# Optimization experiments

Hardware: AMD Instinct MI355X
Metric: run time of the kernel (lower is better)

## Reference

```python
import jax, jax.numpy as jnp
import numpy as np

# --- static configuration (mirrors init_kwargs) ---
L = 16        # latent_size
HL = 512      # hypernet_layer_size
D = 64        # decoder_layer_size
NDEC = 2      # decoder_n_layers
B, G = 128, 100  # batch, grid (pressure levels)
LOGP_MEAN, LOGP_STD = 0.0, 3.0
T_MEAN, T_STD = 1500.0, 500.0

# decoder layer structure generated by the hypernet
WEIGHT_SIZES = [(1, D)] + [(D, D)] * NDEC + [(D, 1)]
BIAS_SIZES = [1] + [D] * NDEC + [1]
OUT_SIZE = sum(a * b for a, b in WEIGHT_SIZES) + sum(BIAS_SIZES)  # 8450


def setup_inputs() -> dict:
    key = jax.random.key(0)
    ks = jax.random.split(key, 8)
    def init(k, shape, fan_in):
        return (jax.random.normal(k, shape, jnp.float32) / np.float32(np.sqrt(fan_in)))
    return {
        "z": jax.random.normal(ks[0], (B, L), jnp.float32),
        "log_P": jax.random.normal(ks[1], (B, G), jnp.float32) * 2.0,
        # hypernet MLP params: L -> HL -> HL -> HL -> OUT_SIZE
        "hW0": init(ks[2], (L, HL), L), "hb0": jnp.zeros((HL,), jnp.float32),
        "hW1": init(ks[3], (HL, HL), HL), "hb1": jnp.zeros((HL,), jnp.float32),
        "hW2": init(ks[4], (HL, HL), HL), "hb2": jnp.zeros((HL,), jnp.float32),
        "hWo": init(ks[5], (HL, OUT_SIZE), HL), "hbo": jnp.zeros((OUT_SIZE,), jnp.float32),
    }


def reference(z, log_P, hW0, hb0, hW1, hb1, hW2, hb2, hWo, hbo):
    Bsz, Gsz = log_P.shape
    R = Bsz * Gsz  # flattened rows
    # broadcast latent over the pressure grid: (B, L) -> (R, L)
    z_flat = jnp.broadcast_to(z[:, None, :], (Bsz, Gsz, z.shape[-1])).reshape(R, -1)
    # normalize pressure -> decoder input, shape (R, 1)
    x = (log_P.reshape(R, 1) - LOGP_MEAN) / LOGP_STD
    # hypernet MLP (leaky_relu, slope 0.01 like torch default)
    h = jax.nn.leaky_relu(z_flat @ hW0 + hb0)
    h = jax.nn.leaky_relu(h @ hW1 + hb1)
    h = jax.nn.leaky_relu(h @ hW2 + hb2)
    wab = h @ hWo + hbo  # (R, OUT_SIZE): per-row decoder weights+biases
    # per-row decoder: chain of batched GEMVs with siren activation
    off = 0
    n_layers = len(WEIGHT_SIZES)
    for i, ((di, do), bs) in enumerate(zip(WEIGHT_SIZES, BIAS_SIZES)):
        n = di * do
        w = wab[:, off:off + n].reshape(R, di, do)
        b = wab[:, off + n:off + n + bs]  # broadcasts against (R, do)
        off += n + bs
        x = jnp.einsum('bi,bij->bj', x, w) + b
        if i == 0:
            x = x * 30.0  # siren first-layer omega_0
        if i < n_layers - 1:
            x = jnp.sin(x)  # siren activation; last layer is Identity
    T_pred = x.reshape(Bsz, Gsz)
    # undo temperature normalization
    return T_pred * T_STD + T_MEAN
```

## Files before the change

kernel.cpp:

```cpp
#include <hip/hip_runtime.h>

#define WSTRIDE 8704
#define GSTR 65

__device__ __forceinline__ float lrelu(float x) { return x > 0.0f ? x : 0.01f * x; }

__global__ __launch_bounds__(128) void h0T_kernel(const float* __restrict__ z,
                                                  const float* __restrict__ W,
                                                  const float* __restrict__ bias,
                                                  float* __restrict__ h0T) {
    int j = blockIdx.x;
    int b = threadIdx.x;
    float zr[16];
    *(float4*)&zr[0]  = *(const float4*)&z[b * 16 + 0];
    *(float4*)&zr[4]  = *(const float4*)&z[b * 16 + 4];
    *(float4*)&zr[8]  = *(const float4*)&z[b * 16 + 8];
    *(float4*)&zr[12] = *(const float4*)&z[b * 16 + 12];
    float acc = bias[j];
#pragma unroll
    for (int l = 0; l < 16; ++l) acc = fmaf(zr[l], W[l * 512 + j], acc);
    h0T[j * 128 + b] = lrelu(acc);
}

__global__ __launch_bounds__(512) void gemmT_kernel(const float* __restrict__ At,
                                                    const float* __restrict__ W,
                                                    const float* __restrict__ bias,
                                                    float* __restrict__ OT) {
    __shared__ __align__(16) float As[512][4];
    __shared__ float red[8][64][5];
    int jt = blockIdx.x & 7;
    int bt = blockIdx.x >> 3;
    int tid = threadIdx.x;
    int lane = tid & 63;
    int wid  = __builtin_amdgcn_readfirstlane(tid >> 6);
    int b0 = bt * 4;
#pragma unroll
    for (int r = 0; r < 2; ++r) {
        int p = r * 512 + tid;
        int k = p >> 1, q = p & 1;
        *(float2*)&As[k][q * 2] = *(const float2*)&At[k * 128 + b0 + q * 2];
    }
    __syncthreads();
    int j = jt * 64 + lane;
    float acc[4] = {};
    int k0 = wid * 64;
#pragma unroll 8
    for (int kk = 0; kk < 64; ++kk) {
        int k = k0 + kk;
        float4 a = *(const float4*)&As[k][0];
        float w = W[k * 512 + j];
        acc[0] = fmaf(a.x, w, acc[0]);
        acc[1] = fmaf(a.y, w, acc[1]);
        acc[2] = fmaf(a.z, w, acc[2]);
        acc[3] = fmaf(a.w, w, acc[3]);
    }
#pragma unroll
    for (int i = 0; i < 4; ++i) red[wid][lane][i] = acc[i];
    __syncthreads();
    if (tid < 256) {
        int jj = tid >> 2;
        int bb = tid & 3;
        float s = 0.f;
#pragma unroll
        for (int w = 0; w < 8; ++w) s += red[w][jj][bb];
        int jg = jt * 64 + jj;
        OT[jg * 128 + b0 + bb] = lrelu(s + bias[jg]);
    }
}

__device__ __forceinline__ void loadg(const float As[][16], const float* __restrict__ W,
                                      int k0, int g, int j0,
                                      float4 (&aa)[4][4], float2 (&ww)[4]) {
    int kb = k0 + g * 4;
#pragma unroll
    for (int kk = 0; kk < 4; ++kk) {
        const float* asr = As[kb + kk];
        aa[kk][0] = *(const float4*)&asr[0];
        aa[kk][1] = *(const float4*)&asr[4];
        aa[kk][2] = *(const float4*)&asr[8];
        aa[kk][3] = *(const float4*)&asr[12];
        ww[kk] = *(const float2*)&W[(kb + kk) * 8450 + j0];
    }
}

__device__ __forceinline__ void compg(const float4 (&aa)[4][4], const float2 (&ww)[4],
                                      float (&acc)[16][2]) {
#pragma unroll
    for (int kk = 0; kk < 4; ++kk) {
#pragma unroll
        for (int q = 0; q < 4; ++q) {
            const float4 a = aa[kk][q];
            const float av[4] = {a.x, a.y, a.z, a.w};
#pragma unroll
            for (int e = 0; e < 4; ++e) {
                acc[q * 4 + e][0] = fmaf(av[e], ww[kk].x, acc[q * 4 + e][0]);
                acc[q * 4 + e][1] = fmaf(av[e], ww[kk].y, acc[q * 4 + e][1]);
            }
        }
    }
}

__global__ __launch_bounds__(256, 2) void wabT_kernel(const float* __restrict__ At,
                                                      const float* __restrict__ W,
                                                      const float* __restrict__ bias,
                                                      float* __restrict__ wab) {
    __shared__ __align__(16) float As[512][16];
    __shared__ float red[4][64][33];
    int tid = threadIdx.x;
    int v = (blockIdx.x & 7) * 67 + (blockIdx.x >> 3);
    int jt = v >> 3;
    int bt = v & 7;
    int lane = tid & 63;
    int wid  = __builtin_amdgcn_readfirstlane(tid >> 6);
    int b0 = bt * 16;
#pragma unroll
    for (int r = 0; r < 16; ++r) {
        int p = r * 256 + tid;
        int k = p >> 3, q = p & 7;
        *(float2*)&As[k][q * 2] = *(const float2*)&At[k * 128 + b0 + q * 2];
    }
    __syncthreads();
    int j0r = jt * 128 + lane * 2;
    int j0 = j0r < 8448 ? j0r : 8448;
    float acc[16][2] = {};
    int k0 = wid * 128;
    float4 aA[4][4], aB[4][4];
    float2 wA[4], wB[4];
    loadg(As, W, k0, 0, j0, aA, wA);
    for (int it = 0; it < 15; ++it) {
        loadg(As, W, k0, 2 * it + 1, j0, aB, wB);
        compg(aA, wA, acc);
        loadg(As, W, k0, 2 * it + 2, j0, aA, wA);
        compg(aB, wB, acc);
    }
    loadg(As, W, k0, 31, j0, aB, wB);
    compg(aA, wA, acc);
    compg(aB, wB, acc);
#pragma unroll
    for (int bb = 0; bb < 16; ++bb) {
        red[wid][lane][bb * 2 + 0] = acc[bb][0];
        red[wid][lane][bb * 2 + 1] = acc[bb][1];
    }
    __syncthreads();
    int jj = tid >> 1;
    int bh = tid & 1;
    int lane_r = jj >> 1;
    int jl = jj & 1;
    int jg = jt * 128 + jj;
    if (jg < 8450) {
        float bj = bias[jg];
#pragma unroll
        for (int bq = 0; bq < 8; ++bq) {
            int bb = bh * 8 + bq;
            int idx = bb * 2 + jl;
            float s = red[0][lane_r][idx] + red[1][lane_r][idx]
                    + red[2][lane_r][idx] + red[3][lane_r][idx];
            wab[(b0 + bb) * WSTRIDE + jg] = s + bj;
        }
    }
}

__global__ __launch_bounds__(512) void decoder_kernel(const float* __restrict__ wab,
                                                      const float* __restrict__ logP,
                                                      float* __restrict__ out) {
    __shared__ __align__(16) float Wl[64 * 64];
    __shared__ float hX[64 * GSTR];
    __shared__ float hY[64 * GSTR];
    __shared__ float red[8][68];
    int b   = blockIdx.x >> 1;
    int gbl = blockIdx.x & 1;
    int tid = threadIdx.x;
    int lane = tid & 63;
    int wid  = __builtin_amdgcn_readfirstlane(tid >> 6);
    int jq = wid * 8;
    int g = gbl * 64 + lane;
    bool act = g < 100;
    const float* __restrict__ row = wab + b * WSTRIDE;
    float x0 = act ? logP[b * 100 + g] * (1.0f / 3.0f) : 0.0f;

    float c0 = row[64];
#pragma unroll
    for (int t = 0; t < 8; ++t)
        hX[(jq + t) * GSTR + lane] = __sinf(30.0f * fmaf(x0, row[jq + t], c0));
#pragma unroll
    for (int r = 0; r < 8; ++r) {
        int idx = r * 512 + tid;
        Wl[idx] = row[65 + idx];
    }
    __syncthreads();

    {
        float a[8];
#pragma unroll
        for (int t = 0; t < 8; ++t) a[t] = row[4161 + jq + t];
#pragma unroll 8
        for (int i = 0; i < 64; ++i) {
            float hi = hX[i * GSTR + lane];
            const float* wr = &Wl[i * 64 + jq];
            float4 w0 = *(const float4*)&wr[0];
            float4 w1 = *(const float4*)&wr[4];
            a[0] = fmaf(hi, w0.x, a[0]);  a[1] = fmaf(hi, w0.y, a[1]);
            a[2] = fmaf(hi, w0.z, a[2]);  a[3] = fmaf(hi, w0.w, a[3]);
            a[4] = fmaf(hi, w1.x, a[4]);  a[5] = fmaf(hi, w1.y, a[5]);
            a[6] = fmaf(hi, w1.z, a[6]);  a[7] = fmaf(hi, w1.w, a[7]);
        }
#pragma unroll
        for (int t = 0; t < 8; ++t) hY[(jq + t) * GSTR + lane] = __sinf(a[t]);
    }
    __syncthreads();
#pragma unroll
    for (int r = 0; r < 8; ++r) {
        int idx = r * 512 + tid;
        Wl[idx] = row[4225 + idx];
    }
    __syncthreads();

    {
        float a[8];
#pragma unroll
        for (int t = 0; t < 8; ++t) a[t] = row[8321 + jq + t];
#pragma unroll 8
        for (int i = 0; i < 64; ++i) {
            float hi = hY[i * GSTR + lane];
            const float* wr = &Wl[i * 64 + jq];
            float4 w0 = *(const float4*)&wr[0];
            float4 w1 = *(const float4*)&wr[4];
            a[0] = fmaf(hi, w0.x, a[0]);  a[1] = fmaf(hi, w0.y, a[1]);
            a[2] = fmaf(hi, w0.z, a[2]);  a[3] = fmaf(hi, w0.w, a[3]);
            a[4] = fmaf(hi, w1.x, a[4]);  a[5] = fmaf(hi, w1.y, a[5]);
            a[6] = fmaf(hi, w1.z, a[6]);  a[7] = fmaf(hi, w1.w, a[7]);
        }
#pragma unroll
        for (int t = 0; t < 8; ++t) hX[(jq + t) * GSTR + lane] = __sinf(a[t]);
    }
    __syncthreads();

    float p = 0.f;
#pragma unroll
    for (int t = 0; t < 8; ++t)
        p = fmaf(hX[(jq + t) * GSTR + lane], row[8385 + jq + t], p);
    red[wid][lane] = p;
    __syncthreads();
    if (wid == 0 && act) {
        float s = row[8449];
#pragma unroll
        for (int w = 0; w < 8; ++w) s += red[w][lane];
        out[b * 100 + g] = fmaf(s, 500.0f, 1500.0f);
    }
}

extern "C" void kernel_launch(void* const* d_in, const int* in_sizes, int n_in,
                              void* d_out, int out_size, void* d_ws, size_t ws_size,
                              hipStream_t stream) {
    const float* z    = (const float*)d_in[0];
    const float* logP = (const float*)d_in[1];
    const float* hW0  = (const float*)d_in[2];
    const float* hb0  = (const float*)d_in[3];
    const float* hW1  = (const float*)d_in[4];
    const float* hb1  = (const float*)d_in[5];
    const float* hW2  = (const float*)d_in[6];
    const float* hb2  = (const float*)d_in[7];
    const float* hWo  = (const float*)d_in[8];
    const float* hbo  = (const float*)d_in[9];
    float* out = (float*)d_out;

    float* wab = (float*)d_ws;
    float* h0T = wab + 128 * WSTRIDE;
    float* h1T = h0T + 512 * 128;
    float* h2T = h1T + 512 * 128;

    h0T_kernel<<<512, 128, 0, stream>>>(z, hW0, hb0, h0T);
    gemmT_kernel<<<256, 512, 0, stream>>>(h0T, hW1, hb1, h1T);
    gemmT_kernel<<<256, 512, 0, stream>>>(h1T, hW2, hb2, h2T);
    wabT_kernel<<<536, 256, 0, stream>>>(h2T, hWo, hbo, wab);
    decoder_kernel<<<256, 512, 0, stream>>>(wab, logP, out);
}
```

Baseline: 61.08 us.

## Shrink wab GEMM batch tile, pad wab rows, decoder reads weights directly

The wab GEMM now uses 8-batch tiles instead of 16, launching twice as many blocks with a simpler unpipelined k loop and fewer registers per thread. Its output is written with a 3-float shift after the first-layer entries, which 16-byte aligns the decoder's 64x64 weight matrices inside each row. The decoder then reads those weights straight from global memory with float4 loads instead of staging them in shared memory, dropping two barriers and the staging copies. The trade-off is that the decoder reuses weights from L1/L2 across waves rather than from LDS, and the GEMM loses its software prefetch and reads the hWo matrix more times.

```diff
diff --git a/kernel.cpp b/kernel.cpp
--- a/kernel.cpp
+++ b/kernel.cpp
@@ -1,7 +1,6 @@
 #include <hip/hip_runtime.h>
 
 #define WSTRIDE 8704
-#define GSTR 65
 
 __device__ __forceinline__ float lrelu(float x) { return x > 0.0f ? x : 0.01f * x; }
 
@@ -68,94 +67,64 @@
     }
 }
 
-__device__ __forceinline__ void loadg(const float As[][16], const float* __restrict__ W,
-                                      int k0, int g, int j0,
-                                      float4 (&aa)[4][4], float2 (&ww)[4]) {
-    int kb = k0 + g * 4;
-#pragma unroll
-    for (int kk = 0; kk < 4; ++kk) {
-        const float* asr = As[kb + kk];
-        aa[kk][0] = *(const float4*)&asr[0];
-        aa[kk][1] = *(const float4*)&asr[4];
-        aa[kk][2] = *(const float4*)&asr[8];
-        aa[kk][3] = *(const float4*)&asr[12];
-        ww[kk] = *(const float2*)&W[(kb + kk) * 8450 + j0];
-    }
-}
-
-__device__ __forceinline__ void compg(const float4 (&aa)[4][4], const float2 (&ww)[4],
-                                      float (&acc)[16][2]) {
-#pragma unroll
-    for (int kk = 0; kk < 4; ++kk) {
-#pragma unroll
-        for (int q = 0; q < 4; ++q) {
-            const float4 a = aa[kk][q];
-            const float av[4] = {a.x, a.y, a.z, a.w};
-#pragma unroll
-            for (int e = 0; e < 4; ++e) {
-                acc[q * 4 + e][0] = fmaf(av[e], ww[kk].x, acc[q * 4 + e][0]);
-                acc[q * 4 + e][1] = fmaf(av[e], ww[kk].y, acc[q * 4 + e][1]);
-            }
-        }
-    }
-}
-
-__global__ __launch_bounds__(256, 2) void wabT_kernel(const float* __restrict__ At,
-                                                      const float* __restrict__ W,
-                                                      const float* __restrict__ bias,
-                                                      float* __restrict__ wab) {
-    __shared__ __align__(16) float As[512][16];
-    __shared__ float red[4][64][33];
+__global__ __launch_bounds__(256) void wabT_kernel(const float* __restrict__ At,
+                                                   const float* __restrict__ W,
+                                                   const float* __restrict__ bias,
+                                                   float* __restrict__ wab) {
+    __shared__ __align__(16) float smem[4352];
+    float (*As)[8] = (float (*)[8])smem;
     int tid = threadIdx.x;
-    int v = (blockIdx.x & 7) * 67 + (blockIdx.x >> 3);
-    int jt = v >> 3;
-    int bt = v & 7;
     int lane = tid & 63;
-    int wid  = __builtin_amdgcn_readfirstlane(tid >> 6);
-    int b0 = bt * 16;
-#pragma unroll
-    for (int r = 0; r < 16; ++r) {
+    int wid = __builtin_amdgcn_readfirstlane(tid >> 6);
+    int jt = blockIdx.x >> 4;
+    int bt = blockIdx.x & 15;
+    if (jt >= 67) return;
+    int b0 = bt * 8;
+#pragma unroll
+    for (int r = 0; r < 8; ++r) {
         int p = r * 256 + tid;
-        int k = p >> 3, q = p & 7;
-        *(float2*)&As[k][q * 2] = *(const float2*)&At[k * 128 + b0 + q * 2];
+        int k = p >> 1, h = (p & 1) * 4;
+        *(float4*)&As[k][h] = *(const float4*)&At[k * 128 + b0 + h];
     }
     __syncthreads();
     int j0r = jt * 128 + lane * 2;
-    int j0 = j0r < 8448 ? j0r : 8448;
-    float acc[16][2] = {};
+    int j0 = j0r <= 8448 ? j0r : 8448;
     int k0 = wid * 128;
-    float4 aA[4][4], aB[4][4];
-    float2 wA[4], wB[4];
-    loadg(As, W, k0, 0, j0, aA, wA);
-    for (int it = 0; it < 15; ++it) {
-        loadg(As, W, k0, 2 * it + 1, j0, aB, wB);
-        compg(aA, wA, acc);
-        loadg(As, W, k0, 2 * it + 2, j0, aA, wA);
-        compg(aB, wB, acc);
-    }
-    loadg(As, W, k0, 31, j0, aB, wB);
-    compg(aA, wA, acc);
-    compg(aB, wB, acc);
-#pragma unroll
-    for (int bb = 0; bb < 16; ++bb) {
-        red[wid][lane][bb * 2 + 0] = acc[bb][0];
-        red[wid][lane][bb * 2 + 1] = acc[bb][1];
-    }
-    __syncthreads();
-    int jj = tid >> 1;
-    int bh = tid & 1;
-    int lane_r = jj >> 1;
-    int jl = jj & 1;
-    int jg = jt * 128 + jj;
+    const float* __restrict__ Wp = W + (size_t)k0 * 8450 + j0;
+    float acc[8][2];
+#pragma unroll
+    for (int i = 0; i < 8; ++i) { acc[i][0] = 0.f; acc[i][1] = 0.f; }
+#pragma unroll 4
+    for (int kk = 0; kk < 128; ++kk) {
+        float4 aL = *(const float4*)&As[k0 + kk][0];
+        float4 aH = *(const float4*)&As[k0 + kk][4];
+        float2 w = *(const float2*)(Wp + (size_t)kk * 8450);
+        float av[8] = {aL.x, aL.y, aL.z, aL.w, aH.x, aH.y, aH.z, aH.w};
+#pragma unroll
+        for (int i = 0; i < 8; ++i) {
+            acc[i][0] = fmaf(av[i], w.x, acc[i][0]);
+            acc[i][1] = fmaf(av[i], w.y, acc[i][1]);
+        }
+    }
+    __syncthreads();
+#pragma unroll
+    for (int i = 0; i < 8; ++i) {
+        smem[(wid * 8 + i) * 132 + lane * 2 + 0] = acc[i][0];
+        smem[(wid * 8 + i) * 132 + lane * 2 + 1] = acc[i][1];
+    }
+    __syncthreads();
+    int j = tid & 127;
+    int bs = tid >> 7;
+    int jg = jt * 128 + j;
     if (jg < 8450) {
         float bj = bias[jg];
-#pragma unroll
-        for (int bq = 0; bq < 8; ++bq) {
-            int bb = bh * 8 + bq;
-            int idx = bb * 2 + jl;
-            float s = red[0][lane_r][idx] + red[1][lane_r][idx]
-                    + red[2][lane_r][idx] + red[3][lane_r][idx];
-            wab[(b0 + bb) * WSTRIDE + jg] = s + bj;
+        int dst = jg + (jg >= 65 ? 3 : 0);
+#pragma unroll
+        for (int q = 0; q < 4; ++q) {
+            int bb = bs * 4 + q;
+            float s = smem[(0 * 8 + bb) * 132 + j] + smem[(1 * 8 + bb) * 132 + j]
+                    + smem[(2 * 8 + bb) * 132 + j] + smem[(3 * 8 + bb) * 132 + j];
+            wab[(size_t)(b0 + bb) * WSTRIDE + dst] = s + bj;
         }
     }
 }
@@ -163,40 +132,31 @@
 __global__ __launch_bounds__(512) void decoder_kernel(const float* __restrict__ wab,
                                                       const float* __restrict__ logP,
                                                       float* __restrict__ out) {
-    __shared__ __align__(16) float Wl[64 * 64];
-    __shared__ float hX[64 * GSTR];
-    __shared__ float hY[64 * GSTR];
+    __shared__ float hX[64 * 65];
+    __shared__ float hY[64 * 65];
     __shared__ float red[8][68];
-    int b   = blockIdx.x >> 1;
-    int gbl = blockIdx.x & 1;
+    int b  = blockIdx.x >> 1;
+    int gh = blockIdx.x & 1;
     int tid = threadIdx.x;
     int lane = tid & 63;
-    int wid  = __builtin_amdgcn_readfirstlane(tid >> 6);
-    int jq = wid * 8;
-    int g = gbl * 64 + lane;
+    int jq = (tid >> 6) * 8;
+    int g = gh * 64 + lane;
     bool act = g < 100;
-    const float* __restrict__ row = wab + b * WSTRIDE;
+    const float* __restrict__ row = wab + (size_t)b * WSTRIDE;
     float x0 = act ? logP[b * 100 + g] * (1.0f / 3.0f) : 0.0f;
-
     float c0 = row[64];
 #pragma unroll
     for (int t = 0; t < 8; ++t)
-        hX[(jq + t) * GSTR + lane] = __sinf(30.0f * fmaf(x0, row[jq + t], c0));
-#pragma unroll
-    for (int r = 0; r < 8; ++r) {
-        int idx = r * 512 + tid;
-        Wl[idx] = row[65 + idx];
-    }
-    __syncthreads();
-
+        hX[(jq + t) * 65 + lane] = __sinf(30.0f * fmaf(x0, row[jq + t], c0));
+    __syncthreads();
     {
         float a[8];
 #pragma unroll
-        for (int t = 0; t < 8; ++t) a[t] = row[4161 + jq + t];
-#pragma unroll 8
+        for (int t = 0; t < 8; ++t) a[t] = row[4164 + jq + t];
+#pragma unroll 4
         for (int i = 0; i < 64; ++i) {
-            float hi = hX[i * GSTR + lane];
-            const float* wr = &Wl[i * 64 + jq];
+            float hi = hX[i * 65 + lane];
+            const float* wr = row + 68 + i * 64 + jq;
             float4 w0 = *(const float4*)&wr[0];
             float4 w1 = *(const float4*)&wr[4];
             a[0] = fmaf(hi, w0.x, a[0]);  a[1] = fmaf(hi, w0.y, a[1]);
@@ -205,24 +165,17 @@
             a[6] = fmaf(hi, w1.z, a[6]);  a[7] = fmaf(hi, w1.w, a[7]);
         }
 #pragma unroll
-        for (int t = 0; t < 8; ++t) hY[(jq + t) * GSTR + lane] = __sinf(a[t]);
-    }
-    __syncthreads();
-#pragma unroll
-    for (int r = 0; r < 8; ++r) {
-        int idx = r * 512 + tid;
-        Wl[idx] = row[4225 + idx];
-    }
-    __syncthreads();
-
+        for (int t = 0; t < 8; ++t) hY[(jq + t) * 65 + lane] = __sinf(a[t]);
+    }
+    __syncthreads();
     {
         float a[8];
 #pragma unroll
-        for (int t = 0; t < 8; ++t) a[t] = row[8321 + jq + t];
-#pragma unroll 8
+        for (int t = 0; t < 8; ++t) a[t] = row[8324 + jq + t];
+#pragma unroll 4
         for (int i = 0; i < 64; ++i) {
-            float hi = hY[i * GSTR + lane];
-            const float* wr = &Wl[i * 64 + jq];
+            float hi = hY[i * 65 + lane];
+            const float* wr = row + 4228 + i * 64 + jq;
             float4 w0 = *(const float4*)&wr[0];
             float4 w1 = *(const float4*)&wr[4];
             a[0] = fmaf(hi, w0.x, a[0]);  a[1] = fmaf(hi, w0.y, a[1]);
@@ -231,18 +184,17 @@
             a[6] = fmaf(hi, w1.z, a[6]);  a[7] = fmaf(hi, w1.w, a[7]);
         }
 #pragma unroll
-        for (int t = 0; t < 8; ++t) hX[(jq + t) * GSTR + lane] = __sinf(a[t]);
-    }
-    __syncthreads();
-
+        for (int t = 0; t < 8; ++t) hX[(jq + t) * 65 + lane] = __sinf(a[t]);
+    }
+    __syncthreads();
     float p = 0.f;
 #pragma unroll
     for (int t = 0; t < 8; ++t)
-        p = fmaf(hX[(jq + t) * GSTR + lane], row[8385 + jq + t], p);
-    red[wid][lane] = p;
-    __syncthreads();
-    if (wid == 0 && act) {
-        float s = row[8449];
+        p = fmaf(hX[(jq + t) * 65 + lane], row[8388 + jq + t], p);
+    red[tid >> 6][lane] = p;
+    __syncthreads();
+    if (tid < 64 && act) {
+        float s = row[8452];
 #pragma unroll
         for (int w = 0; w < 8; ++w) s += red[w][lane];
         out[b * 100 + g] = fmaf(s, 500.0f, 1500.0f);
@@ -272,6 +224,6 @@
     h0T_kernel<<<512, 128, 0, stream>>>(z, hW0, hb0, h0T);
     gemmT_kernel<<<256, 512, 0, stream>>>(h0T, hW1, hb1, h1T);
     gemmT_kernel<<<256, 512, 0, stream>>>(h1T, hW2, hb2, h2T);
-    wabT_kernel<<<536, 256, 0, stream>>>(h2T, hWo, hbo, wab);
+    wabT_kernel<<<1088, 256, 0, stream>>>(h2T, hWo, hbo, wab);
     decoder_kernel<<<256, 512, 0, stream>>>(wab, logP, out);
 }
```

Result: slower. 69.18 us (+13.2%).
